# Kernel tuning notes

Measured on AMD Instinct MI355X. Metric: run time of the kernel, lower is better.

Reference implementation:

```python
import jax, jax.numpy as jnp
import numpy as np

N_NODES = 100000
N_EDGES = 1200000
D_IN = 64
D_OUT = 32
BN_EPS = 1e-5


def setup_inputs() -> dict:
    key = jax.random.key(0)
    ks = jax.random.split(key, 8)
    x = jax.random.normal(ks[0], (N_NODES, D_IN), dtype=jnp.float32)
    edge_index = jax.random.randint(ks[1], (2, N_EDGES), 0, N_NODES, dtype=jnp.int64)
    W1s = jax.random.normal(ks[2], (3, D_IN, D_IN), dtype=jnp.float32) * 0.05
    b1s = jax.random.normal(ks[3], (3, D_IN), dtype=jnp.float32) * 0.05
    W2s = jax.random.normal(ks[4], (3, D_IN, D_IN), dtype=jnp.float32) * 0.05
    b2s = jax.random.normal(ks[5], (3, D_IN), dtype=jnp.float32) * 0.05
    gammas = jnp.ones((3, D_IN), dtype=jnp.float32)
    betas = jnp.zeros((3, D_IN), dtype=jnp.float32)
    epss = jnp.zeros((3,), dtype=jnp.float32)  # GINConv train_eps init value 0
    lin_w = jax.random.normal(ks[6], (D_IN, D_OUT), dtype=jnp.float32) * 0.05
    lin_b = jnp.zeros((D_OUT,), dtype=jnp.float32)
    return {"x": x, "edge_index": edge_index, "W1s": W1s, "b1s": b1s,
            "W2s": W2s, "b2s": b2s, "gammas": gammas, "betas": betas,
            "epss": epss, "lin_w": lin_w, "lin_b": lin_b}


def reference(x, edge_index, W1s, b1s, W2s, b2s, gammas, betas, epss, lin_w, lin_b):
    # PyG GINConv (source_to_target): out_i = nn((1+eps)*x_i + sum_{j->i} x_j)
    src = edge_index[0]
    dst = edge_index[1]
    n = x.shape[0]
    h = x
    for i in range(3):
        agg = jax.ops.segment_sum(h[src], dst, num_segments=n)  # [N, d]
        z = (1.0 + epss[i]) * h + agg
        z = jax.nn.relu(z @ W1s[i] + b1s[i])
        z = jax.nn.relu(z @ W2s[i] + b2s[i])
        # BatchNorm1d, training mode (batch statistics, biased variance)
        mu = jnp.mean(z, axis=0)
        var = jnp.var(z, axis=0)
        z = gammas[i] * (z - mu) * jax.lax.rsqrt(var + BN_EPS) + betas[i]
        h = jax.nn.relu(z)  # F.relu after each conv
    return h @ lin_w + lin_b  # [N, D_OUT]
```

## Files before the change

kernel.cpp:

```cpp
#include <hip/hip_runtime.h>
#include <hip/hip_fp16.h>

#define NBMAX 256
#define BCAP  8192
#define CHB   3584

typedef _Float16 half8 __attribute__((ext_vector_type(8)));
typedef float f32x4 __attribute__((ext_vector_type(4)));

__device__ __forceinline__ unsigned short f2h(float f) {
    __half h = __float2half_rn(f);
    return *(unsigned short*)&h;
}

__device__ __forceinline__ int scan256(int v, int* wsum, int* woff) {
    int t = threadIdx.x, lane = t & 63, wv = t >> 6;
    int x = v;
    #pragma unroll
    for (int d = 1; d < 64; d <<= 1) {
        int y = __shfl_up(x, d, 64);
        if (lane >= d) x += y;
    }
    if (lane == 63) wsum[wv] = x;
    __syncthreads();
    if (t == 0) {
        int a = 0;
        #pragma unroll
        for (int i = 0; i < 4; ++i) { woff[i] = a; a += wsum[i]; }
    }
    __syncthreads();
    return x - v + woff[wv];
}

__global__ __launch_bounds__(256) void gin_init(const void* __restrict__ edge,
                                                int* __restrict__ flag,
                                                int* __restrict__ gcount, int nb,
                                                float* __restrict__ stats, int E) {
    int t = threadIdx.x;
    for (int i = t; i < nb; i += 256) gcount[i] = 0;
    for (int i = t; i < 384; i += 256) stats[i] = 0.f;
    if (t == 0) {
        const int* p = (const int*)edge;
        int is64 = 1;
        int m = (E < 64) ? E : 64;
        for (int i = 0; i < m; ++i)
            if (p[2 * i + 1] != 0) is64 = 0;
        *flag = is64;
    }
}

__global__ __launch_bounds__(256) void gin_x16(const float* __restrict__ x,
                                               unsigned short* __restrict__ o, int n16) {
    int i = blockIdx.x * 256 + threadIdx.x;
    if (i >= n16) return;
    float4 v = ((const float4*)x)[i];
    ushort4 u;
    u.x = f2h(v.x); u.y = f2h(v.y); u.z = f2h(v.z); u.w = f2h(v.w);
    ((ushort4*)o)[i] = u;
}

__global__ __launch_bounds__(256) void gin_binscatter(const void* __restrict__ edge,
                                                      const int* __restrict__ flag,
                                                      int* __restrict__ gcount,
                                                      uint2* __restrict__ ebuf, int E, int nb) {
    __shared__ int cnt[NBMAX];
    __shared__ int dlt[NBMAX];
    __shared__ int cur[NBMAX];
    __shared__ int wsum[4], woff[4];
    __shared__ uint2 buf[CHB];
    int t = threadIdx.x;
    int beg = blockIdx.x * CHB;
    int m = E - beg; if (m > CHB) m = CHB;
    if (t < nb) cnt[t] = 0;
    __syncthreads();
    int is64 = *flag;
    for (int j = t; j < m; j += 256) {
        int e = beg + j;
        int d = is64 ? (int)((const long long*)edge)[E + e] : ((const int*)edge)[E + e];
        atomicAdd(&cnt[d >> 9], 1);
    }
    __syncthreads();
    int v = (t < nb) ? cnt[t] : 0;
    int excl = scan256(v, wsum, woff);
    if (t < nb) {
        int gb = v ? atomicAdd(&gcount[t], v) : 0;
        dlt[t] = t * BCAP + gb - excl;
        cur[t] = excl;
    }
    __syncthreads();
    for (int j = t; j < m; j += 256) {
        int e = beg + j;
        int s, d;
        if (is64) {
            s = (int)((const long long*)edge)[e];
            d = (int)((const long long*)edge)[E + e];
        } else {
            s = ((const int*)edge)[e];
            d = ((const int*)edge)[E + e];
        }
        int p = atomicAdd(&cur[d >> 9], 1);
        buf[p] = make_uint2((unsigned)s, (unsigned)d);
    }
    __syncthreads();
    for (int j = t; j < m; j += 256) {
        uint2 ed = buf[j];
        ebuf[j + dlt[(int)(ed.y >> 9)]] = ed;
    }
}

__global__ __launch_bounds__(256) void gin_build(const uint2* __restrict__ ebuf,
                                                 const int* __restrict__ gcount,
                                                 int* __restrict__ rowbeg,
                                                 int* __restrict__ rowend,
                                                 int* __restrict__ col, int n) {
    __shared__ int cnt[512];
    __shared__ int off[512];
    __shared__ int wsum[4], woff[4];
    int b = blockIdx.x, t = threadIdx.x;
    int beg = b * BCAP;
    int end = beg + gcount[b];
    cnt[t] = 0; cnt[t + 256] = 0;
    __syncthreads();
    for (int j = beg + t; j < end; j += 256)
        atomicAdd(&cnt[(int)(ebuf[j].y & 511)], 1);
    __syncthreads();
    int v0 = cnt[2 * t], v1 = cnt[2 * t + 1];
    int ep = scan256(v0 + v1, wsum, woff);
    off[2 * t] = ep;
    off[2 * t + 1] = ep + v0;
    __syncthreads();
    int node0 = b * 512 + 2 * t;
    if (node0 < n) {
        rowbeg[node0] = beg + off[2 * t];
        rowend[node0] = beg + off[2 * t] + v0;
    }
    if (node0 + 1 < n) {
        rowbeg[node0 + 1] = beg + off[2 * t + 1];
        rowend[node0 + 1] = beg + off[2 * t + 1] + v1;
    }
    __syncthreads();
    for (int j = beg + t; j < end; j += 256) {
        uint2 ed = ebuf[j];
        int p = atomicAdd(&off[(int)(ed.y & 511)], 1);
        col[beg + p] = (int)ed.x;
    }
}

template <bool APPLY>
__device__ __forceinline__ void accum8(float* acc, uint4 u,
                                       const float* sc, const float* sh) {
    float v[8];
    float2 f;
    f = __half22float2(*(const __half2*)&u.x); v[0] = f.x; v[1] = f.y;
    f = __half22float2(*(const __half2*)&u.y); v[2] = f.x; v[3] = f.y;
    f = __half22float2(*(const __half2*)&u.z); v[4] = f.x; v[5] = f.y;
    f = __half22float2(*(const __half2*)&u.w); v[6] = f.x; v[7] = f.y;
    #pragma unroll
    for (int j = 0; j < 8; ++j)
        acc[j] += APPLY ? fmaxf(fmaf(v[j], sc[j], sh[j]), 0.f) : v[j];
}

template <bool APPLY>
__device__ __forceinline__ void gather_body(const unsigned short* __restrict__ zb,
                                            const int* __restrict__ rowbeg,
                                            const int* __restrict__ rowend,
                                            const int* __restrict__ col,
                                            const float* __restrict__ epss,
                                            const float* __restrict__ ss,
                                            int layer,
                                            unsigned short* __restrict__ t,
                                            int wid, int qn, int l16) {
    int r = l16 >> 3, c = l16 & 7;
    float sc[8] = {1.f, 1.f, 1.f, 1.f, 1.f, 1.f, 1.f, 1.f};
    float sh[8] = {0.f, 0.f, 0.f, 0.f, 0.f, 0.f, 0.f, 0.f};
    if (APPLY) {
        const float* p = ss + (layer - 1) * 128;
        *(float4*)&sc[0] = *(const float4*)(p + 8 * c);
        *(float4*)&sc[4] = *(const float4*)(p + 8 * c + 4);
        *(float4*)&sh[0] = *(const float4*)(p + 64 + 8 * c);
        *(float4*)&sh[4] = *(const float4*)(p + 64 + 8 * c + 4);
    }
    int r0 = rowbeg[wid], r1 = rowend[wid];
    uint4 su = make_uint4(0, 0, 0, 0);
    if (r == 0) su = *(const uint4*)(zb + (size_t)wid * 64 + 8 * c);

    float acc[8] = {0.f, 0.f, 0.f, 0.f, 0.f, 0.f, 0.f, 0.f};
    for (int base = r0; base < r1; base += 16) {
        int ce = base + l16;
        int ci = col[ce < r1 ? ce : r1 - 1];
        uint4 u[8];
        bool p[8];
        #pragma unroll
        for (int s = 0; s < 8; ++s) {
            int j = 2 * s + r;
            p[s] = (base + j) < r1;
            int idx = __shfl(ci, 16 * qn + j);
            if (p[s]) u[s] = *(const uint4*)(zb + (size_t)idx * 64 + 8 * c);
        }
        #pragma unroll
        for (int s = 0; s < 8; ++s)
            if (p[s]) accum8<APPLY>(acc, u[s], sc, sh);
    }
    #pragma unroll
    for (int j = 0; j < 8; ++j)
        acc[j] += __shfl_xor(acc[j], 8);
    if (r == 0) {
        float e1 = 1.f + epss[layer];
        float s[8];
        float2 f;
        f = __half22float2(*(const __half2*)&su.x); s[0] = f.x; s[1] = f.y;
        f = __half22float2(*(const __half2*)&su.y); s[2] = f.x; s[3] = f.y;
        f = __half22float2(*(const __half2*)&su.z); s[4] = f.x; s[5] = f.y;
        f = __half22float2(*(const __half2*)&su.w); s[6] = f.x; s[7] = f.y;
        #pragma unroll
        for (int j = 0; j < 8; ++j) {
            float v = APPLY ? fmaxf(fmaf(s[j], sc[j], sh[j]), 0.f) : s[j];
            acc[j] = fmaf(e1, v, acc[j]);
        }
        uint4 o;
        o.x = (unsigned)f2h(acc[0]) | ((unsigned)f2h(acc[1]) << 16);
        o.y = (unsigned)f2h(acc[2]) | ((unsigned)f2h(acc[3]) << 16);
        o.z = (unsigned)f2h(acc[4]) | ((unsigned)f2h(acc[5]) << 16);
        o.w = (unsigned)f2h(acc[6]) | ((unsigned)f2h(acc[7]) << 16);
        *(uint4*)(t + (size_t)wid * 64 + 8 * c) = o;
    }
}

__global__ __launch_bounds__(256) void gin_gather(const unsigned short* __restrict__ zb,
                                                  const int* __restrict__ rowbeg,
                                                  const int* __restrict__ rowend,
                                                  const int* __restrict__ col,
                                                  const float* __restrict__ epss,
                                                  const float* __restrict__ ss,
                                                  int layer, int apply,
                                                  unsigned short* __restrict__ t, int n) {
    int gw = (blockIdx.x * 256 + threadIdx.x) >> 6;
    int lane = threadIdx.x & 63;
    int qn = lane >> 4;
    int wid = gw * 4 + qn;
    int l16 = lane & 15;
    if (wid >= n) return;
    if (apply)
        gather_body<true>(zb, rowbeg, rowend, col, epss, ss, layer, t, wid, qn, l16);
    else
        gather_body<false>(zb, rowbeg, rowend, col, epss, ss, layer, t, wid, qn, l16);
}

__global__ __launch_bounds__(256) void gin_mlp(const unsigned short* __restrict__ t_in,
                                               unsigned short* __restrict__ z16,
                                               const float* __restrict__ W1g,
                                               const float* __restrict__ b1g,
                                               const float* __restrict__ W2g,
                                               const float* __restrict__ b2g,
                                               float* __restrict__ stats, int layer, int n) {
    __shared__ _Float16 Wt[2 * 64 * 72];
    __shared__ _Float16 Z1[128 * 72];
    __shared__ float sS[64], sQ[64];
    int tid = threadIdx.x;
    int base = blockIdx.x * 128;
    const float* __restrict__ W1 = W1g + layer * 4096;
    const float* __restrict__ W2 = W2g + layer * 4096;

    for (int i = tid; i < 4096; i += 256) {
        int k = i >> 6, nn = i & 63;
        Wt[nn * 72 + k]        = (_Float16)W1[i];
        Wt[4608 + nn * 72 + k] = (_Float16)W2[i];
    }
    if (tid < 64) { sS[tid] = 0.f; sQ[tid] = 0.f; }
    __syncthreads();

    int lane = tid & 63, wv = tid >> 6;
    int g = lane >> 4, q = lane & 15;
    int n0 = 32 * wv + q;
    int n1 = n0 + 16;

    const _Float16* tp = (const _Float16*)t_in + (size_t)base * 64;
    half8 tb00 = *(const half8*)(tp + (size_t)n0 * 64 + 8 * g);
    half8 tb01 = *(const half8*)(tp + (size_t)n0 * 64 + 32 + 8 * g);
    half8 tb10 = *(const half8*)(tp + (size_t)n1 * 64 + 8 * g);
    half8 tb11 = *(const half8*)(tp + (size_t)n1 * 64 + 32 + 8 * g);

    f32x4 acc[2][4];
    #pragma unroll
    for (int nt = 0; nt < 2; ++nt)
        #pragma unroll
        for (int ft = 0; ft < 4; ++ft)
            acc[nt][ft] = (f32x4){0.f, 0.f, 0.f, 0.f};

    #pragma unroll
    for (int ft = 0; ft < 4; ++ft) {
        half8 a0 = *(const half8*)&Wt[(16 * ft + q) * 72 + 8 * g];
        half8 a1 = *(const half8*)&Wt[(16 * ft + q) * 72 + 32 + 8 * g];
        acc[0][ft] = __builtin_amdgcn_mfma_f32_16x16x32_f16(a0, tb00, acc[0][ft], 0, 0, 0);
        acc[0][ft] = __builtin_amdgcn_mfma_f32_16x16x32_f16(a1, tb01, acc[0][ft], 0, 0, 0);
        acc[1][ft] = __builtin_amdgcn_mfma_f32_16x16x32_f16(a0, tb10, acc[1][ft], 0, 0, 0);
        acc[1][ft] = __builtin_amdgcn_mfma_f32_16x16x32_f16(a1, tb11, acc[1][ft], 0, 0, 0);
    }

    #pragma unroll
    for (int ft = 0; ft < 4; ++ft) {
        float4 b = *(const float4*)(b1g + layer * 64 + 16 * ft + 4 * g);
        #pragma unroll
        for (int nt = 0; nt < 2; ++nt) {
            int node = nt ? n1 : n0;
            float v0 = fmaxf(acc[nt][ft][0] + b.x, 0.f);
            float v1 = fmaxf(acc[nt][ft][1] + b.y, 0.f);
            float v2 = fmaxf(acc[nt][ft][2] + b.z, 0.f);
            float v3 = fmaxf(acc[nt][ft][3] + b.w, 0.f);
            uint2 pk;
            pk.x = (unsigned)f2h(v0) | ((unsigned)f2h(v1) << 16);
            pk.y = (unsigned)f2h(v2) | ((unsigned)f2h(v3) << 16);
            *(uint2*)&Z1[node * 72 + 16 * ft + 4 * g] = pk;
        }
    }

    half8 zb00 = *(const half8*)&Z1[n0 * 72 + 8 * g];
    half8 zb01 = *(const half8*)&Z1[n0 * 72 + 32 + 8 * g];
    half8 zb10 = *(const half8*)&Z1[n1 * 72 + 8 * g];
    half8 zb11 = *(const half8*)&Z1[n1 * 72 + 32 + 8 * g];
    #pragma unroll
    for (int nt = 0; nt < 2; ++nt)
        #pragma unroll
        for (int ft = 0; ft < 4; ++ft)
            acc[nt][ft] = (f32x4){0.f, 0.f, 0.f, 0.f};
    #pragma unroll
    for (int ft = 0; ft < 4; ++ft) {
        half8 a0 = *(const half8*)&Wt[4608 + (16 * ft + q) * 72 + 8 * g];
        half8 a1 = *(const half8*)&Wt[4608 + (16 * ft + q) * 72 + 32 + 8 * g];
        acc[0][ft] = __builtin_amdgcn_mfma_f32_16x16x32_f16(a0, zb00, acc[0][ft], 0, 0, 0);
        acc[0][ft] = __builtin_amdgcn_mfma_f32_16x16x32_f16(a1, zb01, acc[0][ft], 0, 0, 0);
        acc[1][ft] = __builtin_amdgcn_mfma_f32_16x16x32_f16(a0, zb10, acc[1][ft], 0, 0, 0);
        acc[1][ft] = __builtin_amdgcn_mfma_f32_16x16x32_f16(a1, zb11, acc[1][ft], 0, 0, 0);
    }

    #pragma unroll
    for (int ft = 0; ft < 4; ++ft) {
        float4 b = *(const float4*)(b2g + layer * 64 + 16 * ft + 4 * g);
        float s[4] = {0.f, 0.f, 0.f, 0.f};
        float sq[4] = {0.f, 0.f, 0.f, 0.f};
        #pragma unroll
        for (int nt = 0; nt < 2; ++nt) {
            int node = base + (nt ? n1 : n0);
            float v0 = fmaxf(acc[nt][ft][0] + b.x, 0.f);
            float v1 = fmaxf(acc[nt][ft][1] + b.y, 0.f);
            float v2 = fmaxf(acc[nt][ft][2] + b.z, 0.f);
            float v3 = fmaxf(acc[nt][ft][3] + b.w, 0.f);
            if (node < n) {
                s[0] += v0; sq[0] += v0 * v0;
                s[1] += v1; sq[1] += v1 * v1;
                s[2] += v2; sq[2] += v2 * v2;
                s[3] += v3; sq[3] += v3 * v3;
                uint2 pk;
                pk.x = (unsigned)f2h(v0) | ((unsigned)f2h(v1) << 16);
                pk.y = (unsigned)f2h(v2) | ((unsigned)f2h(v3) << 16);
                *(uint2*)(z16 + (size_t)node * 64 + 16 * ft + 4 * g) = pk;
            }
        }
        #pragma unroll
        for (int off = 1; off < 16; off <<= 1) {
            #pragma unroll
            for (int r2 = 0; r2 < 4; ++r2) {
                s[r2] += __shfl_xor(s[r2], off);
                sq[r2] += __shfl_xor(sq[r2], off);
            }
        }
        if (q == 0) {
            #pragma unroll
            for (int r2 = 0; r2 < 4; ++r2) {
                atomicAdd(&sS[16 * ft + 4 * g + r2], s[r2]);
                atomicAdd(&sQ[16 * ft + 4 * g + r2], sq[r2]);
            }
        }
    }
    __syncthreads();
    if (tid < 64) {
        atomicAdd(&stats[layer * 128 + tid], sS[tid]);
        atomicAdd(&stats[layer * 128 + 64 + tid], sQ[tid]);
    }
}

__global__ void gin_bnfin(const float* __restrict__ stats, const float* __restrict__ gammas,
                          const float* __restrict__ betas, float* __restrict__ ss,
                          int layer, float n) {
    int f = threadIdx.x;
    float mu = stats[layer * 128 + f] / n;
    float var = stats[layer * 128 + 64 + f] / n - mu * mu;
    float rs = rsqrtf(var + 1e-5f);
    float g = gammas[layer * 64 + f];
    float b = betas[layer * 64 + f];
    ss[layer * 128 + f] = g * rs;
    ss[layer * 128 + 64 + f] = b - g * rs * mu;
}

__global__ __launch_bounds__(256) void gin_lin(const unsigned short* __restrict__ zin,
                                               const float* __restrict__ stats,
                                               const float* __restrict__ gammas,
                                               const float* __restrict__ betas,
                                               float fN,
                                               const float* __restrict__ lw,
                                               const float* __restrict__ lb,
                                               float* __restrict__ out, int n) {
    __shared__ float Z[128 * 68];
    int tid = threadIdx.x;
    int base = blockIdx.x * 128;
    int cq = (tid & 15) * 4;
    float4 sc4, sh4;
    {
        float t0[4], t1[4];
        #pragma unroll
        for (int j = 0; j < 4; ++j) {
            int f = cq + j;
            float mu  = stats[256 + f] / fN;
            float var = stats[256 + 64 + f] / fN - mu * mu;
            float g   = gammas[128 + f];
            float grs = g * rsqrtf(var + 1e-5f);
            t0[j] = grs;
            t1[j] = betas[128 + f] - grs * mu;
        }
        sc4 = make_float4(t0[0], t0[1], t0[2], t0[3]);
        sh4 = make_float4(t1[0], t1[1], t1[2], t1[3]);
    }
    {
        const ushort4* __restrict__ src = (const ushort4*)(zin + (size_t)base * 64);
        #pragma unroll
        for (int it = 0; it < 8; ++it) {
            int idx4 = it * 256 + tid;
            int row = idx4 >> 4, c = (idx4 & 15) * 4;
            float4 v = make_float4(0.f, 0.f, 0.f, 0.f);
            if (base + row < n) {
                ushort4 u = src[idx4];
                float2 f0 = __half22float2(*(const __half2*)&u.x);
                float2 f1 = __half22float2(*(const __half2*)&u.z);
                v = make_float4(f0.x, f0.y, f1.x, f1.y);
            }
            float4 r;
            r.x = fmaxf(fmaf(v.x, sc4.x, sh4.x), 0.f);
            r.y = fmaxf(fmaf(v.y, sc4.y, sh4.y), 0.f);
            r.z = fmaxf(fmaf(v.z, sc4.z, sh4.z), 0.f);
            r.w = fmaxf(fmaf(v.w, sc4.w, sh4.w), 0.f);
            *(float4*)&Z[row * 68 + c] = r;
        }
    }
    __syncthreads();
    int tx = tid & 7, ty = tid >> 3;
    float acc[4][4];
    {
        float4 b = *(const float4*)(lb + 4 * tx);
        #pragma unroll
        for (int r = 0; r < 4; ++r) {
            acc[r][0] = b.x; acc[r][1] = b.y; acc[r][2] = b.z; acc[r][3] = b.w;
        }
    }
    #pragma unroll 4
    for (int k = 0; k < 64; ++k) {
        float4 w = *(const float4*)(lw + k * 32 + 4 * tx);
        #pragma unroll
        for (int r = 0; r < 4; ++r) {
            float a = Z[(ty + 32 * r) * 68 + k];
            acc[r][0] = fmaf(a, w.x, acc[r][0]);
            acc[r][1] = fmaf(a, w.y, acc[r][1]);
            acc[r][2] = fmaf(a, w.z, acc[r][2]);
            acc[r][3] = fmaf(a, w.w, acc[r][3]);
        }
    }
    #pragma unroll
    for (int r = 0; r < 4; ++r) {
        int row = base + ty + 32 * r;
        if (row < n) {
            float4 v;
            v.x = acc[r][0]; v.y = acc[r][1]; v.z = acc[r][2]; v.w = acc[r][3];
            *(float4*)(out + (size_t)row * 32 + 4 * tx) = v;
        }
    }
}

extern "C" void kernel_launch(void* const* d_in, const int* in_sizes, int n_in,
                              void* d_out, int out_size, void* d_ws, size_t ws_size,
                              hipStream_t stream) {
    const float* x      = (const float*)d_in[0];
    const void*  edge   = d_in[1];
    const float* W1s    = (const float*)d_in[2];
    const float* b1s    = (const float*)d_in[3];
    const float* W2s    = (const float*)d_in[4];
    const float* b2s    = (const float*)d_in[5];
    const float* gammas = (const float*)d_in[6];
    const float* betas  = (const float*)d_in[7];
    const float* epss   = (const float*)d_in[8];
    const float* lin_w  = (const float*)d_in[9];
    const float* lin_b  = (const float*)d_in[10];
    float* out = (float*)d_out;

    const int N = in_sizes[0] / 64;
    const int E = in_sizes[1] / 2;
    const int NB = (N + 511) >> 9;
    const float fN = (float)N;

    char* w = (char*)d_ws;
    auto take = [&](size_t bytes) {
        char* p = w;
        w += (bytes + 255) & ~(size_t)255;
        return p;
    };
    unsigned short* x16 = (unsigned short*)take((size_t)N * 64 * 2);
    unsigned short* hA  = (unsigned short*)take((size_t)N * 64 * 2);
    unsigned short* hB  = (unsigned short*)take((size_t)N * 64 * 2);
    unsigned short* T   = (unsigned short*)take((size_t)N * 64 * 2);
    uint2* ebuf    = (uint2*)take((size_t)NB * BCAP * 8);
    int*   col     = (int*)take((size_t)NB * BCAP * 4);
    int*   rowbeg  = (int*)take((size_t)N * 4);
    int*   rowend  = (int*)take((size_t)N * 4);
    int*   gcount  = (int*)take((size_t)NBMAX * 4);
    float* stats   = (float*)take(3 * 128 * 4);
    float* ss      = (float*)take(3 * 128 * 4);
    int*   flag    = (int*)take(4);

    gin_init<<<1, 256, 0, stream>>>(edge, flag, gcount, NB, stats, E);
    gin_x16<<<(N * 16 + 255) / 256, 256, 0, stream>>>(x, x16, N * 16);
    gin_binscatter<<<(E + CHB - 1) / CHB, 256, 0, stream>>>(edge, flag, gcount, ebuf, E, NB);
    gin_build<<<NB, 256, 0, stream>>>(ebuf, gcount, rowbeg, rowend, col, N);

    const int gGather = (N + 15) / 16;
    const int gMlp    = (N + 127) / 128;

    const unsigned short* zin = x16;
    unsigned short* zout = hA;
    for (int L = 0; L < 3; ++L) {
        gin_gather<<<gGather, 256, 0, stream>>>(zin, rowbeg, rowend, col, epss, ss, L,
                                                (L > 0) ? 1 : 0, T, N);
        gin_mlp<<<gMlp, 256, 0, stream>>>(T, zout, W1s, b1s, W2s, b2s, stats, L, N);
        if (L < 2) gin_bnfin<<<1, 64, 0, stream>>>(stats, gammas, betas, ss, L, fN);
        zin = zout;
        zout = (zout == hA) ? hB : hA;
    }
    gin_lin<<<gMlp, 256, 0, stream>>>(zin, stats, gammas, betas, fN, lin_w, lin_b, out, N);
}
```

Baseline: 322.8 us.

## Fold init into x16, pack edge buffer, finalize BN stats in last MLP block

Merges the one-block init kernel into the fp16 conversion kernel. Packs each binned edge into 32 bits (23-bit source, 9-bit local destination) to halve edge buffer traffic. Removes the separate BN-finalize launches by having the last MLP block, detected with an atomic done counter, compute scale and shift. This cuts three launches and some memory traffic, but relies on node indices fitting in 23 bits and adds a threadfence and counter per block.

```diff
diff --git a/kernel.cpp b/kernel.cpp
--- a/kernel.cpp
+++ b/kernel.cpp
@@ -32,26 +32,28 @@
     return x - v + woff[wv];
 }
 
-__global__ __launch_bounds__(256) void gin_init(const void* __restrict__ edge,
-                                                int* __restrict__ flag,
-                                                int* __restrict__ gcount, int nb,
-                                                float* __restrict__ stats, int E) {
+__global__ __launch_bounds__(256) void gin_x16(const float* __restrict__ x,
+                                               unsigned short* __restrict__ o, int n16,
+                                               const void* __restrict__ edge,
+                                               int* __restrict__ flag,
+                                               int* __restrict__ gcount, int nb,
+                                               float* __restrict__ stats,
+                                               int* __restrict__ done, int E) {
     int t = threadIdx.x;
-    for (int i = t; i < nb; i += 256) gcount[i] = 0;
-    for (int i = t; i < 384; i += 256) stats[i] = 0.f;
-    if (t == 0) {
-        const int* p = (const int*)edge;
-        int is64 = 1;
-        int m = (E < 64) ? E : 64;
-        for (int i = 0; i < m; ++i)
-            if (p[2 * i + 1] != 0) is64 = 0;
-        *flag = is64;
-    }
-}
-
-__global__ __launch_bounds__(256) void gin_x16(const float* __restrict__ x,
-                                               unsigned short* __restrict__ o, int n16) {
-    int i = blockIdx.x * 256 + threadIdx.x;
+    if (blockIdx.x == 0) {
+        for (int i = t; i < nb; i += 256) gcount[i] = 0;
+        for (int i = t; i < 384; i += 256) stats[i] = 0.f;
+        if (t < 3) done[t] = 0;
+        if (t == 0) {
+            const int* p = (const int*)edge;
+            int is64 = 1;
+            int m = (E < 64) ? E : 64;
+            for (int i = 0; i < m; ++i)
+                if (p[2 * i + 1] != 0) is64 = 0;
+            *flag = is64;
+        }
+    }
+    int i = blockIdx.x * 256 + t;
     if (i >= n16) return;
     float4 v = ((const float4*)x)[i];
     ushort4 u;
@@ -62,7 +64,7 @@
 __global__ __launch_bounds__(256) void gin_binscatter(const void* __restrict__ edge,
                                                       const int* __restrict__ flag,
                                                       int* __restrict__ gcount,
-                                                      uint2* __restrict__ ebuf, int E, int nb) {
+                                                      unsigned* __restrict__ ebuf, int E, int nb) {
     __shared__ int cnt[NBMAX];
     __shared__ int dlt[NBMAX];
     __shared__ int cur[NBMAX];
@@ -104,11 +106,12 @@
     __syncthreads();
     for (int j = t; j < m; j += 256) {
         uint2 ed = buf[j];
-        ebuf[j + dlt[(int)(ed.y >> 9)]] = ed;
-    }
-}
-
-__global__ __launch_bounds__(256) void gin_build(const uint2* __restrict__ ebuf,
+        unsigned pk = ed.x | ((ed.y & 511u) << 23);
+        ebuf[j + dlt[(int)(ed.y >> 9)]] = pk;
+    }
+}
+
+__global__ __launch_bounds__(256) void gin_build(const unsigned* __restrict__ ebuf,
                                                  const int* __restrict__ gcount,
                                                  int* __restrict__ rowbeg,
                                                  int* __restrict__ rowend,
@@ -122,7 +125,7 @@
     cnt[t] = 0; cnt[t + 256] = 0;
     __syncthreads();
     for (int j = beg + t; j < end; j += 256)
-        atomicAdd(&cnt[(int)(ebuf[j].y & 511)], 1);
+        atomicAdd(&cnt[(int)(ebuf[j] >> 23)], 1);
     __syncthreads();
     int v0 = cnt[2 * t], v1 = cnt[2 * t + 1];
     int ep = scan256(v0 + v1, wsum, woff);
@@ -140,9 +143,9 @@
     }
     __syncthreads();
     for (int j = beg + t; j < end; j += 256) {
-        uint2 ed = ebuf[j];
-        int p = atomicAdd(&off[(int)(ed.y & 511)], 1);
-        col[beg + p] = (int)ed.x;
+        unsigned e = ebuf[j];
+        int p = atomicAdd(&off[(int)(e >> 23)], 1);
+        col[beg + p] = (int)(e & 0x7FFFFFu);
     }
 }
 
@@ -252,10 +255,16 @@
                                                const float* __restrict__ b1g,
                                                const float* __restrict__ W2g,
                                                const float* __restrict__ b2g,
-                                               float* __restrict__ stats, int layer, int n) {
+                                               float* __restrict__ stats,
+                                               int* __restrict__ done,
+                                               const float* __restrict__ gammas,
+                                               const float* __restrict__ betas,
+                                               float* __restrict__ ss, float fN,
+                                               int layer, int n, int nblocks) {
     __shared__ _Float16 Wt[2 * 64 * 72];
     __shared__ _Float16 Z1[128 * 72];
     __shared__ float sS[64], sQ[64];
+    __shared__ int lastflag;
     int tid = threadIdx.x;
     int base = blockIdx.x * 128;
     const float* __restrict__ W1 = W1g + layer * 4096;
@@ -377,19 +386,25 @@
         atomicAdd(&stats[layer * 128 + tid], sS[tid]);
         atomicAdd(&stats[layer * 128 + 64 + tid], sQ[tid]);
     }
-}
-
-__global__ void gin_bnfin(const float* __restrict__ stats, const float* __restrict__ gammas,
-                          const float* __restrict__ betas, float* __restrict__ ss,
-                          int layer, float n) {
-    int f = threadIdx.x;
-    float mu = stats[layer * 128 + f] / n;
-    float var = stats[layer * 128 + 64 + f] / n - mu * mu;
-    float rs = rsqrtf(var + 1e-5f);
-    float g = gammas[layer * 64 + f];
-    float b = betas[layer * 64 + f];
-    ss[layer * 128 + f] = g * rs;
-    ss[layer * 128 + 64 + f] = b - g * rs * mu;
+    __syncthreads();
+    if (tid == 0) {
+        __threadfence();
+        int old = atomicAdd(&done[layer], 1);
+        lastflag = (old == nblocks - 1) ? 1 : 0;
+    }
+    __syncthreads();
+    if (lastflag && tid < 64) {
+        float sv = __hip_atomic_load(&stats[layer * 128 + tid],
+                                     __ATOMIC_RELAXED, __HIP_MEMORY_SCOPE_AGENT);
+        float qv = __hip_atomic_load(&stats[layer * 128 + 64 + tid],
+                                     __ATOMIC_RELAXED, __HIP_MEMORY_SCOPE_AGENT);
+        float mu = sv / fN;
+        float var = qv / fN - mu * mu;
+        float g2 = gammas[layer * 64 + tid];
+        float grs = g2 * rsqrtf(var + 1e-5f);
+        ss[layer * 128 + tid] = grs;
+        ss[layer * 128 + 64 + tid] = betas[layer * 64 + tid] - grs * mu;
+    }
 }
 
 __global__ __launch_bounds__(256) void gin_lin(const unsigned short* __restrict__ zin,
@@ -505,17 +520,18 @@
     unsigned short* hA  = (unsigned short*)take((size_t)N * 64 * 2);
     unsigned short* hB  = (unsigned short*)take((size_t)N * 64 * 2);
     unsigned short* T   = (unsigned short*)take((size_t)N * 64 * 2);
-    uint2* ebuf    = (uint2*)take((size_t)NB * BCAP * 8);
+    unsigned* ebuf = (unsigned*)take((size_t)NB * BCAP * 4);
     int*   col     = (int*)take((size_t)NB * BCAP * 4);
     int*   rowbeg  = (int*)take((size_t)N * 4);
     int*   rowend  = (int*)take((size_t)N * 4);
     int*   gcount  = (int*)take((size_t)NBMAX * 4);
     float* stats   = (float*)take(3 * 128 * 4);
     float* ss      = (float*)take(3 * 128 * 4);
+    int*   done    = (int*)take(3 * 4);
     int*   flag    = (int*)take(4);
 
-    gin_init<<<1, 256, 0, stream>>>(edge, flag, gcount, NB, stats, E);
-    gin_x16<<<(N * 16 + 255) / 256, 256, 0, stream>>>(x, x16, N * 16);
+    gin_x16<<<(N * 16 + 255) / 256, 256, 0, stream>>>(x, x16, N * 16, edge, flag,
+                                                      gcount, NB, stats, done, E);
     gin_binscatter<<<(E + CHB - 1) / CHB, 256, 0, stream>>>(edge, flag, gcount, ebuf, E, NB);
     gin_build<<<NB, 256, 0, stream>>>(ebuf, gcount, rowbeg, rowend, col, N);
 
@@ -527,8 +543,8 @@
     for (int L = 0; L < 3; ++L) {
         gin_gather<<<gGather, 256, 0, stream>>>(zin, rowbeg, rowend, col, epss, ss, L,
                                                 (L > 0) ? 1 : 0, T, N);
-        gin_mlp<<<gMlp, 256, 0, stream>>>(T, zout, W1s, b1s, W2s, b2s, stats, L, N);
-        if (L < 2) gin_bnfin<<<1, 64, 0, stream>>>(stats, gammas, betas, ss, L, fN);
+        gin_mlp<<<gMlp, 256, 0, stream>>>(T, zout, W1s, b1s, W2s, b2s, stats, done,
+                                          gammas, betas, ss, fN, L, N, gMlp);
         zin = zout;
         zout = (zout == hA) ? hB : hA;
     }
```

Measured after the change: 338.8 us. +5.0%, slower.
